# Optimization experiments

Hardware: AMD Instinct MI355X
Metric: run time of the kernel (lower is better)

Reference implementation:

```python
import jax, jax.numpy as jnp
import numpy as np

N_NODES = 100000
N_EDGES = 1600000
DIM_IN, DIM_H, DIM_OUT = 128, 128, 64


def setup_inputs() -> dict:
    key = jax.random.key(0)
    ks = jax.random.split(key, 8)
    s = 0.05
    return {
        "x": jax.random.normal(ks[0], (N_NODES, DIM_IN), jnp.float32),
        "edge_index": jax.random.randint(ks[1], (2, N_EDGES), 0, N_NODES, jnp.int64),
        "W_l1": jax.random.normal(ks[2], (DIM_IN, DIM_H), jnp.float32) * s,
        "W_r1": jax.random.normal(ks[3], (DIM_IN, DIM_H), jnp.float32) * s,
        "b1": jax.random.normal(ks[4], (DIM_H,), jnp.float32) * s,
        "W_l2": jax.random.normal(ks[5], (DIM_H, DIM_OUT), jnp.float32) * s,
        "W_r2": jax.random.normal(ks[6], (DIM_H, DIM_OUT), jnp.float32) * s,
        "b2": jax.random.normal(ks[7], (DIM_OUT,), jnp.float32) * s,
    }


def _sage_conv(h, src, dst, n_nodes, W_l, W_r, b):
    # mean-aggregate neighbor features: gather x[src], scatter-sum to dst, divide by in-degree
    msg = h[src]                                              # [E, d]
    agg = jax.ops.segment_sum(msg, dst, num_segments=n_nodes)  # [N, d]
    deg = jax.ops.segment_sum(jnp.ones((src.shape[0],), h.dtype), dst, num_segments=n_nodes)
    mean = agg / jnp.maximum(deg, 1.0)[:, None]
    # out = lin_l(mean) + lin_r(x) ; bias lives on lin_l (PyG SAGEConv default)
    return mean @ W_l + h @ W_r + b


def reference(x, edge_index, W_l1, W_r1, b1, W_l2, W_r2, b2):
    src, dst = edge_index[0], edge_index[1]
    n = x.shape[0]
    h = jax.nn.relu(_sage_conv(x, src, dst, n, W_l1, W_r1, b1))
    # dropout(p=0.5) is identity in eval mode
    return _sage_conv(h, src, dst, n, W_l2, W_r2, b2)
```

## Files before the change

### kernel.cpp

```cpp
#include <hip/hip_runtime.h>

#define NN 100000
#define NE 1600000

typedef __attribute__((ext_vector_type(8))) short bf16x8;
typedef __attribute__((ext_vector_type(4))) float f32x4;

__device__ __forceinline__ float bf2f(unsigned short b) {
    union { unsigned int u; float f; } v;
    v.u = ((unsigned int)b) << 16;
    return v.f;
}
__device__ __forceinline__ unsigned short f2bf(float f) {
    union { float f; unsigned int u; } v; v.f = f;
    unsigned int u = v.u;
    return (unsigned short)((u + 0x7FFFu + ((u >> 16) & 1u)) >> 16);
}

__global__ void detect_kernel(const int* __restrict__ e, int* __restrict__ flag) {
    int t = blockIdx.x * blockDim.x + threadIdx.x;
    if (t < 4096 && e[2 * t + 1] != 0) atomicOr(flag, 1);
}

__device__ __forceinline__ int esrc(const int* e, int mode, int i) {
    return mode ? e[i] : e[2 * i];
}
__device__ __forceinline__ int edst(const int* e, int mode, int i) {
    return mode ? e[NE + i] : e[2 * (NE + i)];
}

#define NRANGE 4
#define RSZ 25000
#define NCHUNK 64
#define EPC (NE / NCHUNK)
#define GS 100352

__global__ __launch_bounds__(1024) void histA_kernel(
    const int* __restrict__ e, const int* __restrict__ flag, int* __restrict__ G) {
    __shared__ int lh[RSZ];
    const int bid = blockIdx.x;
    const int r = bid & (NRANGE - 1);
    const int c = bid >> 2;
    const int lo = r * RSZ;
    for (int idx = threadIdx.x; idx < RSZ; idx += 1024) lh[idx] = 0;
    __syncthreads();
    const int mode = *flag;
    const int base = c * EPC;
    for (int i = base + threadIdx.x; i < base + EPC; i += 1024) {
        int dl = edst(e, mode, i) - lo;
        if ((unsigned)dl < (unsigned)RSZ) atomicAdd(&lh[dl], 1);
    }
    __syncthreads();
    for (int idx = threadIdx.x; idx < RSZ; idx += 1024)
        G[(size_t)c * GS + lo + idx] = lh[idx];
}

__global__ __launch_bounds__(1024) void scatterC_kernel(
    const int* __restrict__ e, const int* __restrict__ flag,
    const int* __restrict__ S, const int* __restrict__ G, int* __restrict__ csr) {
    __shared__ int sOff[RSZ];
    const int bid = blockIdx.x;
    const int r = bid & (NRANGE - 1);
    const int c = bid >> 2;
    const int lo = r * RSZ;
    for (int idx = threadIdx.x; idx < RSZ; idx += 1024)
        sOff[idx] = S[lo + idx] + G[(size_t)c * GS + lo + idx];
    __syncthreads();
    const int mode = *flag;
    const int base = c * EPC;
    for (int i = base + threadIdx.x; i < base + EPC; i += 1024) {
        int dl = edst(e, mode, i) - lo;
        if ((unsigned)dl < (unsigned)RSZ) {
            int s = esrc(e, mode, i);
            csr[atomicAdd(&sOff[dl], 1)] = s;
        }
    }
}

#define PREF_B 391
#define CVT_G 6250

__global__ __launch_bounds__(256) void prefix_cvt_kernel(
    int* __restrict__ G, int* __restrict__ S,
    const float* __restrict__ xin, unsigned short* __restrict__ xb) {
    if (blockIdx.x < PREF_B) {
        int d = blockIdx.x * 256 + threadIdx.x;
        if (d >= NN) return;
        int run = 0;
#pragma unroll 8
        for (int c = 0; c < NCHUNK; c++) {
            size_t idx = (size_t)c * GS + d;
            int t = G[idx];
            G[idx] = run;
            run += t;
        }
        S[d] = run;
    } else {
        long long i = ((long long)(blockIdx.x - PREF_B) * 256 + threadIdx.x) * 8;
        float4 a = *(const float4*)(xin + i);
        float4 b = *(const float4*)(xin + i + 4);
        bf16x8 rv;
        rv[0] = (short)f2bf(a.x); rv[1] = (short)f2bf(a.y);
        rv[2] = (short)f2bf(a.z); rv[3] = (short)f2bf(a.w);
        rv[4] = (short)f2bf(b.x); rv[5] = (short)f2bf(b.y);
        rv[6] = (short)f2bf(b.z); rv[7] = (short)f2bf(b.w);
        *(bf16x8*)(xb + i) = rv;
    }
}

#define SCAN_G 392

__global__ __launch_bounds__(256) void blocksum_kernel(const int* __restrict__ S,
                                                       int* __restrict__ part) {
    int i = blockIdx.x * 256 + threadIdx.x;
    int v = (i < NN) ? S[i] : 0;
#pragma unroll
    for (int off = 32; off; off >>= 1) v += __shfl_down(v, off, 64);
    __shared__ int wsum[4];
    if ((threadIdx.x & 63) == 0) wsum[threadIdx.x >> 6] = v;
    __syncthreads();
    if (threadIdx.x == 0)
        part[blockIdx.x] = wsum[0] + wsum[1] + wsum[2] + wsum[3];
}

__global__ __launch_bounds__(512) void partscan_kernel(int* __restrict__ part) {
    __shared__ int lds[512];
    const int t = threadIdx.x;
    int v = (t < SCAN_G) ? part[t] : 0;
    lds[t] = v;
    __syncthreads();
    for (int off = 1; off < 512; off <<= 1) {
        int u = (t >= off) ? lds[t - off] : 0;
        __syncthreads();
        lds[t] += u;
        __syncthreads();
    }
    if (t < SCAN_G) part[t] = lds[t] - v;
}

__global__ __launch_bounds__(256) void scanfin_kernel(int* __restrict__ S,
                                                      const int* __restrict__ part) {
    __shared__ int lds[256];
    const int t = threadIdx.x;
    const int i = blockIdx.x * 256 + t;
    int v = (i < NN) ? S[i] : 0;
    lds[t] = v;
    __syncthreads();
    for (int off = 1; off < 256; off <<= 1) {
        int u = (t >= off) ? lds[t - off] : 0;
        __syncthreads();
        lds[t] += u;
        __syncthreads();
    }
    if (i < NN) S[i] = lds[t] - v + part[blockIdx.x];
}

__global__ __launch_bounds__(256) void gather_mean128(
    const unsigned short* __restrict__ feat, const int* __restrict__ csr,
    const int* __restrict__ S, unsigned short* __restrict__ out) {
    const int tid = threadIdx.x;
    const int node = blockIdx.x * 16 + (tid >> 4);
    const int c = tid & 15;
    if (node >= NN) return;
    const int begin = S[node];
    const int end = (node == NN - 1) ? NE : S[node + 1];
    float acc0[8] = {0.f, 0.f, 0.f, 0.f, 0.f, 0.f, 0.f, 0.f};
    float acc1[8] = {0.f, 0.f, 0.f, 0.f, 0.f, 0.f, 0.f, 0.f};
    int j = begin;
    for (; j + 4 <= end; j += 4) {
        int s0 = csr[j], s1 = csr[j + 1], s2 = csr[j + 2], s3 = csr[j + 3];
        bf16x8 v0 = *(const bf16x8*)(feat + (size_t)s0 * 128 + 8 * c);
        bf16x8 v1 = *(const bf16x8*)(feat + (size_t)s1 * 128 + 8 * c);
        bf16x8 v2 = *(const bf16x8*)(feat + (size_t)s2 * 128 + 8 * c);
        bf16x8 v3 = *(const bf16x8*)(feat + (size_t)s3 * 128 + 8 * c);
#pragma unroll
        for (int q = 0; q < 8; q++) {
            acc0[q] += bf2f((unsigned short)v0[q]) + bf2f((unsigned short)v2[q]);
            acc1[q] += bf2f((unsigned short)v1[q]) + bf2f((unsigned short)v3[q]);
        }
    }
    for (; j < end; j++) {
        int s = csr[j];
        bf16x8 v = *(const bf16x8*)(feat + (size_t)s * 128 + 8 * c);
#pragma unroll
        for (int q = 0; q < 8; q++) acc0[q] += bf2f((unsigned short)v[q]);
    }
    const float inv = 1.0f / fmaxf((float)(end - begin), 1.0f);
    bf16x8 r;
#pragma unroll
    for (int q = 0; q < 8; q++) r[q] = (short)f2bf((acc0[q] + acc1[q]) * inv);
    *(bf16x8*)(out + (size_t)node * 128 + 8 * c) = r;
}

__global__ __launch_bounds__(256, 2) void mega_gemm(
    const unsigned short* __restrict__ A,
    const unsigned short* __restrict__ X,
    const float* __restrict__ W_l1, const float* __restrict__ W_r1,
    const float* __restrict__ b1,
    const float* __restrict__ W_l2, const float* __restrict__ W_r2,
    const float* __restrict__ b2,
    unsigned short* __restrict__ T2, unsigned short* __restrict__ P3, int N) {
    constexpr int PITCH = 136;
    __shared__ unsigned short sWb[128 * PITCH];
    __shared__ unsigned short sWa[128 * PITCH];

    const int tid = threadIdx.x;
    for (int idx = tid; idx < 128 * 128; idx += 256) {
        int k = idx >> 7, n = idx & 127;
        sWa[n * PITCH + k] = f2bf(W_l1[idx]);
        sWb[n * PITCH + k] = f2bf(W_r1[idx]);
    }
    __syncthreads();

    const int lane = tid & 63;
    const int wv = tid >> 6;
    const int r16 = lane & 15;
    const int kg = lane >> 4;
    const long long rowbase = (long long)blockIdx.x * 128 + wv * 32;

    bf16x8 xf[2][4], af[2][4];
    const bf16x8 zz = {0, 0, 0, 0, 0, 0, 0, 0};
#pragma unroll
    for (int rt = 0; rt < 2; rt++) {
        long long row = rowbase + rt * 16 + r16;
        bool ok = row < N;
#pragma unroll
        for (int ks = 0; ks < 4; ks++) {
            xf[rt][ks] = ok ? *(const bf16x8*)(X + row * 128 + ks * 32 + kg * 8) : zz;
            af[rt][ks] = ok ? *(const bf16x8*)(A + row * 128 + ks * 32 + kg * 8) : zz;
        }
    }

    f32x4 acc[2][8];
#pragma unroll
    for (int t = 0; t < 8; t++) {
        float bv = b1[t * 16 + r16];
#pragma unroll
        for (int rt = 0; rt < 2; rt++) acc[rt][t] = (f32x4){bv, bv, bv, bv};
    }

#pragma unroll
    for (int t = 0; t < 8; t++) {
        const unsigned short* wp = &sWb[(t * 16 + r16) * PITCH + kg * 8];
        const unsigned short* wq = &sWa[(t * 16 + r16) * PITCH + kg * 8];
        bf16x8 bb[4], ba[4];
#pragma unroll
        for (int ks = 0; ks < 4; ks++) {
            bb[ks] = *(const bf16x8*)(wp + ks * 32);
            ba[ks] = *(const bf16x8*)(wq + ks * 32);
        }
#pragma unroll
        for (int rt = 0; rt < 2; rt++) {
#pragma unroll
            for (int ks = 0; ks < 4; ks++) {
                acc[rt][t] = __builtin_amdgcn_mfma_f32_16x16x32_bf16(
                    xf[rt][ks], bb[ks], acc[rt][t], 0, 0, 0);
                acc[rt][t] = __builtin_amdgcn_mfma_f32_16x16x32_bf16(
                    af[rt][ks], ba[ks], acc[rt][t], 0, 0, 0);
            }
        }
    }

    __syncthreads();

    for (int idx = tid; idx < 128 * 64; idx += 256) {
        int k = idx >> 6, n = idx & 63;
        sWa[n * PITCH + k] = f2bf(W_l2[idx]);
        sWa[64 * PITCH + n * PITCH + k] = f2bf(W_r2[idx]);
    }
    unsigned short* sh = sWb + wv * 32 * PITCH;
#pragma unroll
    for (int rt = 0; rt < 2; rt++)
#pragma unroll
        for (int t = 0; t < 8; t++)
#pragma unroll
            for (int r = 0; r < 4; r++)
                sh[(rt * 16 + kg * 4 + r) * PITCH + t * 16 + r16] =
                    f2bf(fmaxf(acc[rt][t][r], 0.f));
    __syncthreads();

    bf16x8 hf[2][4];
#pragma unroll
    for (int rt = 0; rt < 2; rt++)
#pragma unroll
        for (int ks = 0; ks < 4; ks++)
            hf[rt][ks] = *(const bf16x8*)(sh + (rt * 16 + r16) * PITCH + ks * 32 + kg * 8);

    {
        f32x4 o[2][4];
#pragma unroll
        for (int t = 0; t < 4; t++)
#pragma unroll
            for (int rt = 0; rt < 2; rt++) o[rt][t] = (f32x4){0.f, 0.f, 0.f, 0.f};
#pragma unroll
        for (int t = 0; t < 4; t++) {
            const unsigned short* wp = &sWa[(t * 16 + r16) * PITCH + kg * 8];
            bf16x8 bb[4];
#pragma unroll
            for (int ks = 0; ks < 4; ks++) bb[ks] = *(const bf16x8*)(wp + ks * 32);
#pragma unroll
            for (int rt = 0; rt < 2; rt++)
#pragma unroll
                for (int ks = 0; ks < 4; ks++)
                    o[rt][t] = __builtin_amdgcn_mfma_f32_16x16x32_bf16(
                        hf[rt][ks], bb[ks], o[rt][t], 0, 0, 0);
        }
#pragma unroll
        for (int rt = 0; rt < 2; rt++)
#pragma unroll
            for (int r = 0; r < 4; r++) {
                long long row = rowbase + rt * 16 + kg * 4 + r;
                if (row < N)
#pragma unroll
                    for (int t = 0; t < 4; t++)
                        T2[row * 64 + t * 16 + r16] = f2bf(o[rt][t][r]);
            }
    }
    {
        f32x4 o[2][4];
#pragma unroll
        for (int t = 0; t < 4; t++) {
            float bv = b2[t * 16 + r16];
#pragma unroll
            for (int rt = 0; rt < 2; rt++) o[rt][t] = (f32x4){bv, bv, bv, bv};
        }
#pragma unroll
        for (int t = 0; t < 4; t++) {
            const unsigned short* wp = &sWa[64 * PITCH + (t * 16 + r16) * PITCH + kg * 8];
            bf16x8 bb[4];
#pragma unroll
            for (int ks = 0; ks < 4; ks++) bb[ks] = *(const bf16x8*)(wp + ks * 32);
#pragma unroll
            for (int rt = 0; rt < 2; rt++)
#pragma unroll
                for (int ks = 0; ks < 4; ks++)
                    o[rt][t] = __builtin_amdgcn_mfma_f32_16x16x32_bf16(
                        hf[rt][ks], bb[ks], o[rt][t], 0, 0, 0);
        }
#pragma unroll
        for (int rt = 0; rt < 2; rt++)
#pragma unroll
            for (int r = 0; r < 4; r++) {
                long long row = rowbase + rt * 16 + kg * 4 + r;
                if (row < N)
#pragma unroll
                    for (int t = 0; t < 4; t++)
                        P3[row * 64 + t * 16 + r16] = f2bf(o[rt][t][r]);
            }
    }
}

__global__ __launch_bounds__(256) void gather2_fused(
    const unsigned short* __restrict__ t2, const unsigned short* __restrict__ p3,
    const int* __restrict__ csr, const int* __restrict__ S, float* __restrict__ out) {
    const int tid = threadIdx.x;
    const int node = blockIdx.x * 32 + (tid >> 3);
    const int c = tid & 7;
    if (node >= NN) return;
    const int begin = S[node];
    const int end = (node == NN - 1) ? NE : S[node + 1];
    float acc0[8] = {0.f, 0.f, 0.f, 0.f, 0.f, 0.f, 0.f, 0.f};
    float acc1[8] = {0.f, 0.f, 0.f, 0.f, 0.f, 0.f, 0.f, 0.f};
    int j = begin;
    for (; j + 4 <= end; j += 4) {
        int s0 = csr[j], s1 = csr[j + 1], s2 = csr[j + 2], s3 = csr[j + 3];
        bf16x8 v0 = *(const bf16x8*)(t2 + (size_t)s0 * 64 + 8 * c);
        bf16x8 v1 = *(const bf16x8*)(t2 + (size_t)s1 * 64 + 8 * c);
        bf16x8 v2 = *(const bf16x8*)(t2 + (size_t)s2 * 64 + 8 * c);
        bf16x8 v3 = *(const bf16x8*)(t2 + (size_t)s3 * 64 + 8 * c);
#pragma unroll
        for (int q = 0; q < 8; q++) {
            acc0[q] += bf2f((unsigned short)v0[q]) + bf2f((unsigned short)v2[q]);
            acc1[q] += bf2f((unsigned short)v1[q]) + bf2f((unsigned short)v3[q]);
        }
    }
    for (; j < end; j++) {
        int s = csr[j];
        bf16x8 v = *(const bf16x8*)(t2 + (size_t)s * 64 + 8 * c);
#pragma unroll
        for (int q = 0; q < 8; q++) acc0[q] += bf2f((unsigned short)v[q]);
    }
    const float inv = 1.0f / fmaxf((float)(end - begin), 1.0f);
    bf16x8 pv = *(const bf16x8*)(p3 + (size_t)node * 64 + 8 * c);
    f32x4 r0, r1;
#pragma unroll
    for (int q = 0; q < 4; q++) {
        r0[q] = (acc0[q] + acc1[q]) * inv + bf2f((unsigned short)pv[q]);
        r1[q] = (acc0[4 + q] + acc1[4 + q]) * inv + bf2f((unsigned short)pv[4 + q]);
    }
    *(f32x4*)(out + (size_t)node * 64 + 8 * c) = r0;
    *(f32x4*)(out + (size_t)node * 64 + 8 * c + 4) = r1;
}

extern "C" void kernel_launch(void* const* d_in, const int* in_sizes, int n_in,
                              void* d_out, int out_size, void* d_ws, size_t ws_size,
                              hipStream_t stream) {
    const float* x    = (const float*)d_in[0];
    const int*   e32  = (const int*)d_in[1];
    const float* W_l1 = (const float*)d_in[2];
    const float* W_r1 = (const float*)d_in[3];
    const float* b1   = (const float*)d_in[4];
    const float* W_l2 = (const float*)d_in[5];
    const float* W_r2 = (const float*)d_in[6];
    const float* b2   = (const float*)d_in[7];
    float* out = (float*)d_out;

    int* wsI = (int*)d_ws;
    int* flag = wsI;
    int* S    = wsI + 1024;
    int* part = wsI + 101376;
    int* csr  = wsI + 101888;
    unsigned short* xb = (unsigned short*)(wsI + 1701888);
    int* G = wsI + 8101888;
    unsigned short* mean1b = (unsigned short*)(wsI + 8101888);
    unsigned short* t2b    = (unsigned short*)(wsI + 14524416);
    unsigned short* p3b    = (unsigned short*)(wsI + 17724416);

    hipMemsetAsync(d_ws, 0, 4096, stream);

    detect_kernel<<<16, 256, 0, stream>>>(e32, flag);
    histA_kernel<<<NRANGE * NCHUNK, 1024, 0, stream>>>(e32, flag, G);
    prefix_cvt_kernel<<<PREF_B + CVT_G, 256, 0, stream>>>(G, S, x, xb);
    blocksum_kernel<<<SCAN_G, 256, 0, stream>>>(S, part);
    partscan_kernel<<<1, 512, 0, stream>>>(part);
    scanfin_kernel<<<SCAN_G, 256, 0, stream>>>(S, part);
    scatterC_kernel<<<NRANGE * NCHUNK, 1024, 0, stream>>>(e32, flag, S, G, csr);

    gather_mean128<<<6250, 256, 0, stream>>>(xb, csr, S, mean1b);

    mega_gemm<<<782, 256, 0, stream>>>(mean1b, xb, W_l1, W_r1, b1,
                                       W_l2, W_r2, b2, t2b, p3b, NN);

    gather2_fused<<<3125, 256, 0, stream>>>(t2b, p3b, csr, S, out);
}
```

Measured before the change: 206.4 us.

## Split fused GEMM into two kernels with precomputed transposed bf16 weights

Adds a small kernel that converts and transposes all four weight matrices to bf16 once, instead of every GEMM block converting them into shared memory. The fused two-layer GEMM is split into gemm1 (writes the ReLU hidden layer H to global) and gemm23 (reads H and computes both second-layer products). The weight B-fragments are now read straight from global/L2 rather than LDS. This removes the per-block conversion and the LDS staging, but adds a round trip of H through global memory and one more kernel launch. The t2 and p3 buffers now reuse the xb workspace region, which xb no longer needs by that point.

```diff
diff --git a/kernel.cpp b/kernel.cpp
--- a/kernel.cpp
+++ b/kernel.cpp
@@ -27,6 +27,33 @@
 }
 __device__ __forceinline__ int edst(const int* e, int mode, int i) {
     return mode ? e[NE + i] : e[2 * (NE + i)];
+}
+
+__global__ __launch_bounds__(256) void wcvt_kernel(
+    const float* __restrict__ W_l1, const float* __restrict__ W_r1,
+    const float* __restrict__ W_l2, const float* __restrict__ W_r2,
+    unsigned short* __restrict__ wt) {
+    int b = blockIdx.x;
+    const float* src; unsigned short* dst; int NO, tk, tn;
+    if (b < 4)       { src = W_l1; dst = wt;         NO = 128; tk = b >> 1; tn = b & 1; }
+    else if (b < 8)  { b -= 4; src = W_r1; dst = wt + 16384; NO = 128; tk = b >> 1; tn = b & 1; }
+    else if (b < 10) { b -= 8; src = W_l2; dst = wt + 32768; NO = 64; tk = b; tn = 0; }
+    else             { b -= 10; src = W_r2; dst = wt + 40960; NO = 64; tk = b; tn = 0; }
+    __shared__ unsigned short lt[64][72];
+    const int r0 = tk * 64, c0 = tn * 64;
+    const int lr = threadIdx.x >> 6;
+    const int lc = threadIdx.x & 63;
+#pragma unroll
+    for (int i = 0; i < 16; i++) {
+        int r = lr * 16 + i;
+        lt[lc][r] = f2bf(src[(size_t)(r0 + r) * NO + c0 + lc]);
+    }
+    __syncthreads();
+#pragma unroll
+    for (int i = 0; i < 16; i++) {
+        int n = lr * 16 + i;
+        dst[(size_t)(c0 + n) * 128 + r0 + lc] = lt[n][lc];
+    }
 }
 
 #define NRANGE 4
@@ -192,26 +219,14 @@
     *(bf16x8*)(out + (size_t)node * 128 + 8 * c) = r;
 }
 
-__global__ __launch_bounds__(256, 2) void mega_gemm(
+__global__ __launch_bounds__(256) void gemm1_kernel(
     const unsigned short* __restrict__ A,
     const unsigned short* __restrict__ X,
-    const float* __restrict__ W_l1, const float* __restrict__ W_r1,
+    const unsigned short* __restrict__ WaT,
+    const unsigned short* __restrict__ WbT,
     const float* __restrict__ b1,
-    const float* __restrict__ W_l2, const float* __restrict__ W_r2,
-    const float* __restrict__ b2,
-    unsigned short* __restrict__ T2, unsigned short* __restrict__ P3, int N) {
-    constexpr int PITCH = 136;
-    __shared__ unsigned short sWb[128 * PITCH];
-    __shared__ unsigned short sWa[128 * PITCH];
-
+    unsigned short* __restrict__ H, int N) {
     const int tid = threadIdx.x;
-    for (int idx = tid; idx < 128 * 128; idx += 256) {
-        int k = idx >> 7, n = idx & 127;
-        sWa[n * PITCH + k] = f2bf(W_l1[idx]);
-        sWb[n * PITCH + k] = f2bf(W_r1[idx]);
-    }
-    __syncthreads();
-
     const int lane = tid & 63;
     const int wv = tid >> 6;
     const int r16 = lane & 15;
@@ -241,13 +256,13 @@
 
 #pragma unroll
     for (int t = 0; t < 8; t++) {
-        const unsigned short* wp = &sWb[(t * 16 + r16) * PITCH + kg * 8];
-        const unsigned short* wq = &sWa[(t * 16 + r16) * PITCH + kg * 8];
+        const unsigned short* wb = WbT + (size_t)(t * 16 + r16) * 128 + kg * 8;
+        const unsigned short* wa = WaT + (size_t)(t * 16 + r16) * 128 + kg * 8;
         bf16x8 bb[4], ba[4];
 #pragma unroll
         for (int ks = 0; ks < 4; ks++) {
-            bb[ks] = *(const bf16x8*)(wp + ks * 32);
-            ba[ks] = *(const bf16x8*)(wq + ks * 32);
+            bb[ks] = *(const bf16x8*)(wb + ks * 32);
+            ba[ks] = *(const bf16x8*)(wa + ks * 32);
         }
 #pragma unroll
         for (int rt = 0; rt < 2; rt++) {
@@ -261,93 +276,87 @@
         }
     }
 
-    __syncthreads();
-
-    for (int idx = tid; idx < 128 * 64; idx += 256) {
-        int k = idx >> 6, n = idx & 63;
-        sWa[n * PITCH + k] = f2bf(W_l2[idx]);
-        sWa[64 * PITCH + n * PITCH + k] = f2bf(W_r2[idx]);
-    }
-    unsigned short* sh = sWb + wv * 32 * PITCH;
 #pragma unroll
     for (int rt = 0; rt < 2; rt++)
 #pragma unroll
-        for (int t = 0; t < 8; t++)
-#pragma unroll
-            for (int r = 0; r < 4; r++)
-                sh[(rt * 16 + kg * 4 + r) * PITCH + t * 16 + r16] =
-                    f2bf(fmaxf(acc[rt][t][r], 0.f));
-    __syncthreads();
+        for (int r = 0; r < 4; r++) {
+            long long row = rowbase + rt * 16 + kg * 4 + r;
+            if (row < N)
+#pragma unroll
+                for (int t = 0; t < 8; t++)
+                    H[row * 128 + t * 16 + r16] = f2bf(fmaxf(acc[rt][t][r], 0.f));
+        }
+}
+
+__global__ __launch_bounds__(256) void gemm23_kernel(
+    const unsigned short* __restrict__ Hb,
+    const unsigned short* __restrict__ WlT,
+    const unsigned short* __restrict__ WrT,
+    const float* __restrict__ b2,
+    unsigned short* __restrict__ T2, unsigned short* __restrict__ P3, int N) {
+    const int tid = threadIdx.x;
+    const int lane = tid & 63;
+    const int wv = tid >> 6;
+    const int r16 = lane & 15;
+    const int kg = lane >> 4;
+    const long long rowbase = (long long)blockIdx.x * 128 + wv * 32;
 
     bf16x8 hf[2][4];
+    const bf16x8 zz = {0, 0, 0, 0, 0, 0, 0, 0};
+#pragma unroll
+    for (int rt = 0; rt < 2; rt++) {
+        long long row = rowbase + rt * 16 + r16;
+        bool ok = row < N;
+#pragma unroll
+        for (int ks = 0; ks < 4; ks++)
+            hf[rt][ks] = ok ? *(const bf16x8*)(Hb + row * 128 + ks * 32 + kg * 8) : zz;
+    }
+
+    f32x4 ot[2][4], op[2][4];
+#pragma unroll
+    for (int t = 0; t < 4; t++) {
+        float bv = b2[t * 16 + r16];
+#pragma unroll
+        for (int rt = 0; rt < 2; rt++) {
+            ot[rt][t] = (f32x4){0.f, 0.f, 0.f, 0.f};
+            op[rt][t] = (f32x4){bv, bv, bv, bv};
+        }
+    }
+
+#pragma unroll
+    for (int t = 0; t < 4; t++) {
+        const unsigned short* wl = WlT + (size_t)(t * 16 + r16) * 128 + kg * 8;
+        const unsigned short* wr = WrT + (size_t)(t * 16 + r16) * 128 + kg * 8;
+        bf16x8 bl[4], br[4];
+#pragma unroll
+        for (int ks = 0; ks < 4; ks++) {
+            bl[ks] = *(const bf16x8*)(wl + ks * 32);
+            br[ks] = *(const bf16x8*)(wr + ks * 32);
+        }
+#pragma unroll
+        for (int rt = 0; rt < 2; rt++) {
+#pragma unroll
+            for (int ks = 0; ks < 4; ks++) {
+                ot[rt][t] = __builtin_amdgcn_mfma_f32_16x16x32_bf16(
+                    hf[rt][ks], bl[ks], ot[rt][t], 0, 0, 0);
+                op[rt][t] = __builtin_amdgcn_mfma_f32_16x16x32_bf16(
+                    hf[rt][ks], br[ks], op[rt][t], 0, 0, 0);
+            }
+        }
+    }
+
 #pragma unroll
     for (int rt = 0; rt < 2; rt++)
 #pragma unroll
-        for (int ks = 0; ks < 4; ks++)
-            hf[rt][ks] = *(const bf16x8*)(sh + (rt * 16 + r16) * PITCH + ks * 32 + kg * 8);
-
-    {
-        f32x4 o[2][4];
-#pragma unroll
-        for (int t = 0; t < 4; t++)
-#pragma unroll
-            for (int rt = 0; rt < 2; rt++) o[rt][t] = (f32x4){0.f, 0.f, 0.f, 0.f};
-#pragma unroll
-        for (int t = 0; t < 4; t++) {
-            const unsigned short* wp = &sWa[(t * 16 + r16) * PITCH + kg * 8];
-            bf16x8 bb[4];
-#pragma unroll
-            for (int ks = 0; ks < 4; ks++) bb[ks] = *(const bf16x8*)(wp + ks * 32);
-#pragma unroll
-            for (int rt = 0; rt < 2; rt++)
-#pragma unroll
-                for (int ks = 0; ks < 4; ks++)
-                    o[rt][t] = __builtin_amdgcn_mfma_f32_16x16x32_bf16(
-                        hf[rt][ks], bb[ks], o[rt][t], 0, 0, 0);
-        }
-#pragma unroll
-        for (int rt = 0; rt < 2; rt++)
-#pragma unroll
-            for (int r = 0; r < 4; r++) {
-                long long row = rowbase + rt * 16 + kg * 4 + r;
-                if (row < N)
-#pragma unroll
-                    for (int t = 0; t < 4; t++)
-                        T2[row * 64 + t * 16 + r16] = f2bf(o[rt][t][r]);
-            }
-    }
-    {
-        f32x4 o[2][4];
-#pragma unroll
-        for (int t = 0; t < 4; t++) {
-            float bv = b2[t * 16 + r16];
-#pragma unroll
-            for (int rt = 0; rt < 2; rt++) o[rt][t] = (f32x4){bv, bv, bv, bv};
-        }
-#pragma unroll
-        for (int t = 0; t < 4; t++) {
-            const unsigned short* wp = &sWa[64 * PITCH + (t * 16 + r16) * PITCH + kg * 8];
-            bf16x8 bb[4];
-#pragma unroll
-            for (int ks = 0; ks < 4; ks++) bb[ks] = *(const bf16x8*)(wp + ks * 32);
-#pragma unroll
-            for (int rt = 0; rt < 2; rt++)
-#pragma unroll
-                for (int ks = 0; ks < 4; ks++)
-                    o[rt][t] = __builtin_amdgcn_mfma_f32_16x16x32_bf16(
-                        hf[rt][ks], bb[ks], o[rt][t], 0, 0, 0);
-        }
-#pragma unroll
-        for (int rt = 0; rt < 2; rt++)
-#pragma unroll
-            for (int r = 0; r < 4; r++) {
-                long long row = rowbase + rt * 16 + kg * 4 + r;
-                if (row < N)
-#pragma unroll
-                    for (int t = 0; t < 4; t++)
-                        P3[row * 64 + t * 16 + r16] = f2bf(o[rt][t][r]);
-            }
-    }
+        for (int r = 0; r < 4; r++) {
+            long long row = rowbase + rt * 16 + kg * 4 + r;
+            if (row < N)
+#pragma unroll
+                for (int t = 0; t < 4; t++) {
+                    T2[row * 64 + t * 16 + r16] = f2bf(ot[rt][t][r]);
+                    P3[row * 64 + t * 16 + r16] = f2bf(op[rt][t][r]);
+                }
+        }
 }
 
 __global__ __launch_bounds__(256) void gather2_fused(
@@ -411,14 +420,17 @@
     int* part = wsI + 101376;
     int* csr  = wsI + 101888;
     unsigned short* xb = (unsigned short*)(wsI + 1701888);
+    unsigned short* t2b = (unsigned short*)(wsI + 1701888);
+    unsigned short* p3b = (unsigned short*)(wsI + 4901888);
     int* G = wsI + 8101888;
     unsigned short* mean1b = (unsigned short*)(wsI + 8101888);
-    unsigned short* t2b    = (unsigned short*)(wsI + 14524416);
-    unsigned short* p3b    = (unsigned short*)(wsI + 17724416);
+    unsigned short* hb     = (unsigned short*)(wsI + 14524416);
+    unsigned short* wt     = (unsigned short*)(wsI + 20924416);
 
     hipMemsetAsync(d_ws, 0, 4096, stream);
 
     detect_kernel<<<16, 256, 0, stream>>>(e32, flag);
+    wcvt_kernel<<<12, 256, 0, stream>>>(W_l1, W_r1, W_l2, W_r2, wt);
     histA_kernel<<<NRANGE * NCHUNK, 1024, 0, stream>>>(e32, flag, G);
     prefix_cvt_kernel<<<PREF_B + CVT_G, 256, 0, stream>>>(G, S, x, xb);
     blocksum_kernel<<<SCAN_G, 256, 0, stream>>>(S, part);
@@ -428,8 +440,10 @@
 
     gather_mean128<<<6250, 256, 0, stream>>>(xb, csr, S, mean1b);
 
-    mega_gemm<<<782, 256, 0, stream>>>(mean1b, xb, W_l1, W_r1, b1,
-                                       W_l2, W_r2, b2, t2b, p3b, NN);
+    gemm1_kernel<<<782, 256, 0, stream>>>(mean1b, xb, wt, wt + 16384, b1, hb, NN);
+
+    gemm23_kernel<<<782, 256, 0, stream>>>(hb, wt + 32768, wt + 40960, b2,
+                                           t2b, p3b, NN);
 
     gather2_fused<<<3125, 256, 0, stream>>>(t2b, p3b, csr, S, out);
 }
```

Result: slower. 237.3 us (+15.0%).
